# Kernel tuning notes

Measured on AMD Instinct MI355X. Metric: run time of the kernel, lower is better.

Reference implementation:

```python
import jax, jax.numpy as jnp
import numpy as np

E = 800_000          # number of edges
G = 1_000_000        # number of edge groups (pairs of edges)
EDGE_DIM = 128
HIDDEN = 256
HEADS = 8
NUM_NODES = 100_000  # edge_index.max()+1 in the original; fixed constant here


def _lin(key, fan_in, fan_out):
    # torch.nn.Linear default init ~ U(-1/sqrt(fan_in), 1/sqrt(fan_in)); use scaled normal
    s = 1.0 / np.sqrt(fan_in)
    kw, kb = jax.random.split(key)
    W = jax.random.normal(kw, (fan_in, fan_out), dtype=jnp.float32) * s
    b = jax.random.normal(kb, (fan_out,), dtype=jnp.float32) * s
    return W, b


def setup_inputs() -> dict:
    key = jax.random.key(0)
    ks = jax.random.split(key, 9)
    edge_embeddings = jax.random.normal(ks[0], (E, EDGE_DIM), dtype=jnp.float32)
    edge_groups = jax.random.randint(ks[1], (G, 2), 0, E, dtype=jnp.int64)
    edge_index = jax.random.randint(ks[2], (2, E), 0, NUM_NODES, dtype=jnp.int64)
    W1, b1 = _lin(ks[3], 2 * EDGE_DIM, HIDDEN)
    W2, b2 = _lin(ks[4], HIDDEN, HEADS)
    Ws1, bs1 = _lin(ks[5], 4, HIDDEN // 4)
    Ws2, bs2 = _lin(ks[6], HIDDEN // 4, 1)
    Wc1, bc1 = _lin(ks[7], HEADS + 1, HIDDEN // 2)
    Wc2, bc2 = _lin(ks[8], HIDDEN // 2, 1)
    return {
        "edge_embeddings": edge_embeddings, "edge_groups": edge_groups, "edge_index": edge_index,
        "W1": W1, "b1": b1, "W2": W2, "b2": b2,
        "Ws1": Ws1, "bs1": bs1, "Ws2": Ws2, "bs2": bs2,
        "Wc1": Wc1, "bc1": bc1, "Wc2": Wc2, "bc2": bc2,
    }


def reference(edge_embeddings, edge_groups, edge_index,
              W1, b1, W2, b2, Ws1, bs1, Ws2, bs2, Wc1, bc1, Wc2, bc2):
    # --- gather edge-pair embeddings: [G, 2*edge_dim] ---
    pair = jnp.concatenate(
        [edge_embeddings[edge_groups[:, 0]], edge_embeddings[edge_groups[:, 1]]], axis=-1)
    # compatibility scorer: Linear-ReLU-Linear-ReLU -> [G, HEADS]
    comp = jax.nn.relu(jax.nn.relu(pair @ W1 + b1) @ W2 + b2)

    # --- degrees via scatter-add (replaces serial Python loop) ---
    deg = jnp.zeros((NUM_NODES,), dtype=jnp.float32)
    deg = deg.at[edge_index[0]].add(1.0).at[edge_index[1]].add(1.0)

    # structural features: degrees of the 4 endpoint nodes -> [G, 4]
    ni = edge_index[:, edge_groups[:, 0]]  # [2, G]
    nj = edge_index[:, edge_groups[:, 1]]  # [2, G]
    sf = jnp.stack([deg[ni[0]], deg[ni[1]], deg[nj[0]], deg[nj[1]]], axis=-1)
    ss = jax.nn.relu(sf @ Ws1 + bs1) @ Ws2 + bs2  # [G, 1]

    # combine and squash -> [G]
    allscores = jnp.concatenate([comp, ss], axis=-1)  # [G, HEADS+1]
    out = jax.nn.sigmoid(jax.nn.relu(allscores @ Wc1 + bc1) @ Wc2 + bc2)
    return out.squeeze(-1)
```

## Files before the change

kernel.cpp:

```cpp
#include <hip/hip_runtime.h>
#include <math.h>

#define E_CNT 800000
#define G_CNT 1000000
#define NUM_NODES 100000
#define ROWS 128
#define NT ((G_CNT + ROWS - 1) / ROWS)
#define GRID 256
#define TPB 512

typedef __attribute__((ext_vector_type(8))) short bf16x8;
typedef __attribute__((ext_vector_type(4))) float f32x4;
typedef __attribute__((ext_vector_type(16))) float f32x16;

__device__ __forceinline__ short f2bf(float f) {
    union { float f; unsigned u; } v; v.f = f;
    unsigned r = v.u + 0x7fffu + ((v.u >> 16) & 1u);
    return (short)(r >> 16);
}

__global__ void zero_deg_kernel(float* __restrict__ deg) {
    int i = blockIdx.x * blockDim.x + threadIdx.x;
    if (i < NUM_NODES) deg[i] = 0.0f;
}

__global__ void degree_kernel(const int* __restrict__ ei, float* __restrict__ deg) {
    int e = blockIdx.x * blockDim.x + threadIdx.x;
    if (e < E_CNT) {
        atomicAdd(&deg[ei[e]], 1.0f);
        atomicAdd(&deg[ei[E_CNT + e]], 1.0f);
    }
}

__global__ void prep_w1t_kernel(const float* __restrict__ W1, short* __restrict__ w1t) {
    int t = blockIdx.x * blockDim.x + threadIdx.x;
    int n = t >> 8, k = t & 255;
    w1t[t] = f2bf(W1[k * 256 + n]);
}

__global__ void prep_emb_kernel(const float* __restrict__ emb, short* __restrict__ ebf) {
    long t = (long)blockIdx.x * blockDim.x + threadIdx.x;
    const float4* e4 = (const float4*)emb;
    float4 v0 = e4[t * 2], v1 = e4[t * 2 + 1];
    bf16x8 h;
    h[0] = f2bf(v0.x); h[1] = f2bf(v0.y); h[2] = f2bf(v0.z); h[3] = f2bf(v0.w);
    h[4] = f2bf(v1.x); h[5] = f2bf(v1.y); h[6] = f2bf(v1.z); h[7] = f2bf(v1.w);
    *(bf16x8*)&ebf[t * 8] = h;
}

__global__ void tail_kernel(
    const float* __restrict__ compW,
    const int*   __restrict__ eg,
    const int*   __restrict__ ei,
    const float* __restrict__ deg,
    const float* __restrict__ Ws1, const float* __restrict__ bs1,
    const float* __restrict__ Ws2, const float* __restrict__ bs2,
    const float* __restrict__ Wc1, const float* __restrict__ bc1,
    const float* __restrict__ Wc2, const float* __restrict__ bc2,
    float* __restrict__ out)
{
    int g = blockIdx.x * blockDim.x + threadIdx.x;
    if (g >= G_CNT) return;
    int2 gg = ((const int2*)eg)[g];
    float s0 = deg[ei[gg.x]];
    float s1 = deg[ei[E_CNT + gg.x]];
    float s2 = deg[ei[gg.y]];
    float s3 = deg[ei[E_CNT + gg.y]];
    float4 c0 = ((const float4*)compW)[g * 2];
    float4 c1 = ((const float4*)compW)[g * 2 + 1];
    float cc[8] = {c0.x, c0.y, c0.z, c0.w, c1.x, c1.y, c1.z, c1.w};

    float ss = bs2[0];
    #pragma unroll 8
    for (int u = 0; u < 64; ++u) {
        float h = bs1[u] + s0 * Ws1[u] + s1 * Ws1[64 + u]
                         + s2 * Ws1[128 + u] + s3 * Ws1[192 + u];
        ss += fmaxf(h, 0.f) * Ws2[u];
    }
    float p = bc2[0];
    #pragma unroll 8
    for (int u = 0; u < 128; ++u) {
        float h = bc1[u] + ss * Wc1[1024 + u];
        #pragma unroll
        for (int a = 0; a < 8; ++a) h += cc[a] * Wc1[a * 128 + u];
        p += fmaxf(h, 0.f) * Wc2[u];
    }
    out[g] = 1.f / (1.f + expf(-p));
}

template <int MODE>
__launch_bounds__(TPB, 2)
__global__ void egis_main_kernel(
    const float* __restrict__ emb,
    const int*   __restrict__ eg,
    const float* __restrict__ b1,
    const float* __restrict__ W2, const float* __restrict__ b2,
    const short* __restrict__ w1t,
    const short* __restrict__ ebf,
    float* __restrict__ compW)
{
    __shared__ short pairS[2][ROWS][256];
    __shared__ short w2tS[16][264];
    __shared__ int   gS[2][2][ROWS];

    const int tid = threadIdx.x;
    const int wv = tid >> 6, lane = tid & 63;
    const int l32 = lane & 31, lh32 = lane >> 5;
    const int axr32 = l32 & 7;
    const int l16 = lane & 15, lh = lane >> 4;
    const int axr16 = l16 & 7;

    bf16x8 bReg[16];
    {
        const bf16x8* B8 = (const bf16x8*)w1t;
        const int bBase = (wv * 32 + l32) * 32 + lh32;
        #pragma unroll
        for (int ks = 0; ks < 16; ++ks) bReg[ks] = B8[bBase + ks * 2];
    }
    const float b1v = b1[wv * 32 + l32];
    const float b2v = (l16 < 8) ? b2[l16] : 0.f;

    for (int i = tid; i < 2048; i += TPB) w2tS[i & 7][i >> 3] = f2bf(W2[i]);
    for (int i = tid; i < (8 * 264) / 2; i += TPB) ((int*)&w2tS[8][0])[i] = 0;
    __syncthreads();

    int t = blockIdx.x;
    if (tid < ROWS) {
        int gid = t * ROWS + tid; if (gid >= G_CNT) gid = G_CNT - 1;
        int2 g = ((const int2*)eg)[gid];
        gS[0][0][tid] = g.x; gS[0][1][tid] = g.y;
    }
    __syncthreads();

    if constexpr (MODE == 2) {
        short* dst = &pairS[0][0][0];
        #pragma unroll
        for (int it = 0; it < 8; ++it) {
            int idx = it * TPB + tid;
            int r = idx >> 5, rc = idx & 31;
            int gi = rc ^ (r & 7);
            int grow = (gi & 16) ? gS[0][1][r] : gS[0][0][r];
            const short* src = ebf + (long)grow * 128 + (gi & 15) * 8;
            __builtin_amdgcn_global_load_lds(
                (const __attribute__((address_space(1))) void*)src,
                (__attribute__((address_space(3))) void*)(dst + idx * 8), 16, 0, 0);
        }
    } else {
        #pragma unroll 2
        for (int it = 0; it < 8; ++it) {
            int idx = it * TPB + tid;
            int r = idx >> 5, rc = idx & 31;
            int gi = rc ^ (r & 7);
            int grow = (gi & 16) ? gS[0][1][r] : gS[0][0][r];
            const float4* s4 = (const float4*)(emb + (long)grow * 128 + (gi & 15) * 8);
            float4 v0 = s4[0], v1 = s4[1];
            bf16x8 h;
            h[0] = f2bf(v0.x); h[1] = f2bf(v0.y); h[2] = f2bf(v0.z); h[3] = f2bf(v0.w);
            h[4] = f2bf(v1.x); h[5] = f2bf(v1.y); h[6] = f2bf(v1.z); h[7] = f2bf(v1.w);
            *(bf16x8*)&pairS[0][r][rc * 8] = h;
        }
    }
    int2 egReg = {0, 0};
    {
        int tn = (t + GRID < NT) ? t + GRID : NT - 1;
        if (tid < ROWS) {
            int gid = tn * ROWS + tid; if (gid >= G_CNT) gid = G_CNT - 1;
            egReg = ((const int2*)eg)[gid];
        }
    }

    int cur = 0;
    while (t < NT) {
        const int nxt = cur ^ 1;

        if (tid < ROWS) { gS[nxt][0][tid] = egReg.x; gS[nxt][1][tid] = egReg.y; }
        __syncthreads();

        if constexpr (MODE == 2) {
            short* dst = &pairS[nxt][0][0];
            #pragma unroll
            for (int it = 0; it < 8; ++it) {
                int idx = it * TPB + tid;
                int r = idx >> 5, rc = idx & 31;
                int gi = rc ^ (r & 7);
                int grow = (gi & 16) ? gS[nxt][1][r] : gS[nxt][0][r];
                const short* src = ebf + (long)grow * 128 + (gi & 15) * 8;
                __builtin_amdgcn_global_load_lds(
                    (const __attribute__((address_space(1))) void*)src,
                    (__attribute__((address_space(3))) void*)(dst + idx * 8), 16, 0, 0);
            }
        } else {
            #pragma unroll 2
            for (int it = 0; it < 8; ++it) {
                int idx = it * TPB + tid;
                int r = idx >> 5, rc = idx & 31;
                int gi = rc ^ (r & 7);
                int grow = (gi & 16) ? gS[nxt][1][r] : gS[nxt][0][r];
                const float4* s4 = (const float4*)(emb + (long)grow * 128 + (gi & 15) * 8);
                float4 v0 = s4[0], v1 = s4[1];
                bf16x8 h;
                h[0] = f2bf(v0.x); h[1] = f2bf(v0.y); h[2] = f2bf(v0.z); h[3] = f2bf(v0.w);
                h[4] = f2bf(v1.x); h[5] = f2bf(v1.y); h[6] = f2bf(v1.z); h[7] = f2bf(v1.w);
                *(bf16x8*)&pairS[nxt][r][rc * 8] = h;
            }
        }
        {
            int tn2 = (t + 2 * GRID < NT) ? t + 2 * GRID : NT - 1;
            if (tid < ROWS) {
                int gid = tn2 * ROWS + tid; if (gid >= G_CNT) gid = G_CNT - 1;
                egReg = ((const int2*)eg)[gid];
            }
        }

        f32x16 acc0, acc1, acc2, acc3;
        #pragma unroll
        for (int i = 0; i < 16; ++i) { acc0[i] = b1v; acc1[i] = b1v; acc2[i] = b1v; acc3[i] = b1v; }
        {
            const short* r0 = &pairS[cur][ 0 + l32][0];
            const short* r1 = &pairS[cur][32 + l32][0];
            const short* r2 = &pairS[cur][64 + l32][0];
            const short* r3 = &pairS[cur][96 + l32][0];
            #pragma unroll
            for (int ks = 0; ks < 16; ++ks) {
                int off = ((ks * 2 + lh32) ^ axr32) * 8;
                bf16x8 a0 = *(const bf16x8*)(r0 + off);
                bf16x8 a1 = *(const bf16x8*)(r1 + off);
                bf16x8 a2 = *(const bf16x8*)(r2 + off);
                bf16x8 a3 = *(const bf16x8*)(r3 + off);
                acc0 = __builtin_amdgcn_mfma_f32_32x32x16_bf16(a0, bReg[ks], acc0, 0, 0, 0);
                acc1 = __builtin_amdgcn_mfma_f32_32x32x16_bf16(a1, bReg[ks], acc1, 0, 0, 0);
                acc2 = __builtin_amdgcn_mfma_f32_32x32x16_bf16(a2, bReg[ks], acc2, 0, 0, 0);
                acc3 = __builtin_amdgcn_mfma_f32_32x32x16_bf16(a3, bReg[ks], acc3, 0, 0, 0);
            }
        }
        __syncthreads();

        {
            int col = wv * 32 + l32;
            #pragma unroll
            for (int g = 0; g < 4; ++g) {
                #pragma unroll
                for (int i = 0; i < 4; ++i) {
                    int rb = g * 8 + lh32 * 4 + i;
                    int sw0 = ((rb & 7) << 3);
                    pairS[cur][  0 + rb][col ^ sw0] = f2bf(fmaxf(acc0[g * 4 + i], 0.f));
                    pairS[cur][ 32 + rb][col ^ sw0] = f2bf(fmaxf(acc1[g * 4 + i], 0.f));
                    pairS[cur][ 64 + rb][col ^ sw0] = f2bf(fmaxf(acc2[g * 4 + i], 0.f));
                    pairS[cur][ 96 + rb][col ^ sw0] = f2bf(fmaxf(acc3[g * 4 + i], 0.f));
                }
            }
        }
        __syncthreads();

        {
            f32x4 a2c = (f32x4){b2v, b2v, b2v, b2v};
            const short* hRow = &pairS[cur][wv * 16 + l16][0];
            const bf16x8* w2c = (const bf16x8*)&w2tS[0][0];
            const int wb = l16 * 33 + lh;
            #pragma unroll
            for (int ks = 0; ks < 8; ++ks) {
                bf16x8 a = *(const bf16x8*)(hRow + ((ks * 4 + lh) ^ axr16) * 8);
                bf16x8 b = w2c[wb + ks * 4];
                a2c = __builtin_amdgcn_mfma_f32_16x16x32_bf16(a, b, a2c, 0, 0, 0);
            }
            if (l16 < 8) {
                long base = (long)t * ROWS + wv * 16;
                #pragma unroll
                for (int i = 0; i < 4; ++i)
                    compW[(base + lh * 4 + i) * 8 + l16] = fmaxf(a2c[i], 0.f);
            }
        }

        cur = nxt;
        t += GRID;
    }
}

extern "C" void kernel_launch(void* const* d_in, const int* in_sizes, int n_in,
                              void* d_out, int out_size, void* d_ws, size_t ws_size,
                              hipStream_t stream) {
    const float* emb = (const float*)d_in[0];
    const int*   eg  = (const int*)d_in[1];
    const int*   ei  = (const int*)d_in[2];
    const float* W1  = (const float*)d_in[3];
    const float* b1  = (const float*)d_in[4];
    const float* W2  = (const float*)d_in[5];
    const float* b2  = (const float*)d_in[6];
    const float* Ws1 = (const float*)d_in[7];
    const float* bs1 = (const float*)d_in[8];
    const float* Ws2 = (const float*)d_in[9];
    const float* bs2 = (const float*)d_in[10];
    const float* Wc1 = (const float*)d_in[11];
    const float* bc1 = (const float*)d_in[12];
    const float* Wc2 = (const float*)d_in[13];
    const float* bc2 = (const float*)d_in[14];
    float* out = (float*)d_out;

    char* p = (char*)d_ws;
    float* deg = (float*)p;
    size_t degB = ((size_t)NUM_NODES * 4 + 255) & ~(size_t)255;
    short* w1t = (short*)(p + degB);
    size_t w1tB = 256 * 256 * sizeof(short);
    float* compW = (float*)(p + degB + w1tB);
    size_t compB = (size_t)NT * ROWS * 8 * sizeof(float);
    short* ebf = (short*)(p + degB + w1tB + compB);
    size_t embB = (size_t)E_CNT * 128 * sizeof(short);

    int mode = (ws_size >= degB + w1tB + compB + embB) ? 2
             : (ws_size >= degB + w1tB + compB) ? 1 : 1;

    zero_deg_kernel<<<(NUM_NODES + 255) / 256, 256, 0, stream>>>(deg);
    degree_kernel<<<(E_CNT + 255) / 256, 256, 0, stream>>>(ei, deg);
    prep_w1t_kernel<<<65536 / 256, 256, 0, stream>>>(W1, w1t);
    if (mode == 2) {
        prep_emb_kernel<<<50000, 256, 0, stream>>>(emb, ebf);
        egis_main_kernel<2><<<GRID, TPB, 0, stream>>>(
            emb, eg, b1, W2, b2, w1t, ebf, compW);
    } else {
        egis_main_kernel<1><<<GRID, TPB, 0, stream>>>(
            emb, eg, b1, W2, b2, w1t, (const short*)nullptr, compW);
    }
    tail_kernel<<<(G_CNT + 255) / 256, 256, 0, stream>>>(
        compW, eg, ei, deg, Ws1, bs1, Ws2, bs2, Wc1, bc1, Wc2, bc2, out);
}
```

Before: 463.3 us.

## Fuse prep kernels into one launch and store comp scores column-major

Folds the degree scatter, W1 transpose and embedding bf16 conversion into a single block-partitioned kernel, which removes two launches and lets the independent preprocessing jobs run concurrently. It also changes the intermediate comp-score buffer from row-major [G,8] to head-major [8,G]. The main kernel then writes 16-byte vector stores per head, and the tail kernel reads coalesced per-head columns instead of 32-byte rows. The cost is eight separate strided streams in the tail kernel in place of one contiguous stream.

New measurement: 451.3 us, median of 2. 1.03x faster.

```diff
diff --git a/kernel.cpp b/kernel.cpp
--- a/kernel.cpp
+++ b/kernel.cpp
@@ -6,6 +6,7 @@
 #define NUM_NODES 100000
 #define ROWS 128
 #define NT ((G_CNT + ROWS - 1) / ROWS)
+#define CSTRIDE ((size_t)NT * ROWS)
 #define GRID 256
 #define TPB 512
 
@@ -24,28 +25,38 @@
     if (i < NUM_NODES) deg[i] = 0.0f;
 }
 
-__global__ void degree_kernel(const int* __restrict__ ei, float* __restrict__ deg) {
-    int e = blockIdx.x * blockDim.x + threadIdx.x;
-    if (e < E_CNT) {
-        atomicAdd(&deg[ei[e]], 1.0f);
-        atomicAdd(&deg[ei[E_CNT + e]], 1.0f);
-    }
-}
-
-__global__ void prep_w1t_kernel(const float* __restrict__ W1, short* __restrict__ w1t) {
-    int t = blockIdx.x * blockDim.x + threadIdx.x;
-    int n = t >> 8, k = t & 255;
-    w1t[t] = f2bf(W1[k * 256 + n]);
-}
-
-__global__ void prep_emb_kernel(const float* __restrict__ emb, short* __restrict__ ebf) {
-    long t = (long)blockIdx.x * blockDim.x + threadIdx.x;
-    const float4* e4 = (const float4*)emb;
-    float4 v0 = e4[t * 2], v1 = e4[t * 2 + 1];
-    bf16x8 h;
-    h[0] = f2bf(v0.x); h[1] = f2bf(v0.y); h[2] = f2bf(v0.z); h[3] = f2bf(v0.w);
-    h[4] = f2bf(v1.x); h[5] = f2bf(v1.y); h[6] = f2bf(v1.z); h[7] = f2bf(v1.w);
-    *(bf16x8*)&ebf[t * 8] = h;
+#define PREP_EMB_BLOCKS 50000
+#define PREP_DEG_BLOCKS 3125
+#define PREP_W1T_BLOCKS 256
+template <bool DOEMB>
+__global__ void prep_fused_kernel(
+    const float* __restrict__ emb, short* __restrict__ ebf,
+    const int* __restrict__ ei, float* __restrict__ deg,
+    const float* __restrict__ W1, short* __restrict__ w1t)
+{
+    int b = blockIdx.x;
+    if (DOEMB && b < PREP_EMB_BLOCKS) {
+        long t = (long)b * 256 + threadIdx.x;
+        const float4* e4 = (const float4*)emb;
+        float4 v0 = e4[t * 2], v1 = e4[t * 2 + 1];
+        bf16x8 h;
+        h[0] = f2bf(v0.x); h[1] = f2bf(v0.y); h[2] = f2bf(v0.z); h[3] = f2bf(v0.w);
+        h[4] = f2bf(v1.x); h[5] = f2bf(v1.y); h[6] = f2bf(v1.z); h[7] = f2bf(v1.w);
+        *(bf16x8*)&ebf[t * 8] = h;
+        return;
+    }
+    int b2 = DOEMB ? (b - PREP_EMB_BLOCKS) : b;
+    if (b2 < PREP_DEG_BLOCKS) {
+        int e = b2 * 256 + threadIdx.x;
+        if (e < E_CNT) {
+            atomicAdd(&deg[ei[e]], 1.0f);
+            atomicAdd(&deg[ei[E_CNT + e]], 1.0f);
+        }
+    } else {
+        int t = (b2 - PREP_DEG_BLOCKS) * 256 + threadIdx.x;
+        int n = t >> 8, k = t & 255;
+        w1t[t] = f2bf(W1[k * 256 + n]);
+    }
 }
 
 __global__ void tail_kernel(
@@ -66,9 +77,9 @@
     float s1 = deg[ei[E_CNT + gg.x]];
     float s2 = deg[ei[gg.y]];
     float s3 = deg[ei[E_CNT + gg.y]];
-    float4 c0 = ((const float4*)compW)[g * 2];
-    float4 c1 = ((const float4*)compW)[g * 2 + 1];
-    float cc[8] = {c0.x, c0.y, c0.z, c0.w, c1.x, c1.y, c1.z, c1.w};
+    float cc[8];
+    #pragma unroll
+    for (int a = 0; a < 8; ++a) cc[a] = compW[a * CSTRIDE + g];
 
     float ss = bs2[0];
     #pragma unroll 8
@@ -264,10 +275,11 @@
                 a2c = __builtin_amdgcn_mfma_f32_16x16x32_bf16(a, b, a2c, 0, 0, 0);
             }
             if (l16 < 8) {
-                long base = (long)t * ROWS + wv * 16;
-                #pragma unroll
-                for (int i = 0; i < 4; ++i)
-                    compW[(base + lh * 4 + i) * 8 + l16] = fmaxf(a2c[i], 0.f);
+                long base = (long)t * ROWS + wv * 16 + lh * 4;
+                f32x4 v;
+                v[0] = fmaxf(a2c[0], 0.f); v[1] = fmaxf(a2c[1], 0.f);
+                v[2] = fmaxf(a2c[2], 0.f); v[3] = fmaxf(a2c[3], 0.f);
+                *(f32x4*)&compW[(size_t)l16 * CSTRIDE + base] = v;
             }
         }
 
@@ -302,21 +314,21 @@
     short* w1t = (short*)(p + degB);
     size_t w1tB = 256 * 256 * sizeof(short);
     float* compW = (float*)(p + degB + w1tB);
-    size_t compB = (size_t)NT * ROWS * 8 * sizeof(float);
+    size_t compB = 8 * CSTRIDE * sizeof(float);
     short* ebf = (short*)(p + degB + w1tB + compB);
     size_t embB = (size_t)E_CNT * 128 * sizeof(short);
 
-    int mode = (ws_size >= degB + w1tB + compB + embB) ? 2
-             : (ws_size >= degB + w1tB + compB) ? 1 : 1;
+    int mode = (ws_size >= degB + w1tB + compB + embB) ? 2 : 1;
 
     zero_deg_kernel<<<(NUM_NODES + 255) / 256, 256, 0, stream>>>(deg);
-    degree_kernel<<<(E_CNT + 255) / 256, 256, 0, stream>>>(ei, deg);
-    prep_w1t_kernel<<<65536 / 256, 256, 0, stream>>>(W1, w1t);
     if (mode == 2) {
-        prep_emb_kernel<<<50000, 256, 0, stream>>>(emb, ebf);
+        prep_fused_kernel<true><<<PREP_EMB_BLOCKS + PREP_DEG_BLOCKS + PREP_W1T_BLOCKS,
+                                  256, 0, stream>>>(emb, ebf, ei, deg, W1, w1t);
         egis_main_kernel<2><<<GRID, TPB, 0, stream>>>(
             emb, eg, b1, W2, b2, w1t, ebf, compW);
     } else {
+        prep_fused_kernel<false><<<PREP_DEG_BLOCKS + PREP_W1T_BLOCKS,
+                                   256, 0, stream>>>(emb, (short*)nullptr, ei, deg, W1, w1t);
         egis_main_kernel<1><<<GRID, TPB, 0, stream>>>(
             emb, eg, b1, W2, b2, w1t, (const short*)nullptr, compW);
     }
```
